# Kernel optimization log

Measured on AMD Instinct MI355X. Metric: run time of the kernel, lower is better.

The kernel has to match this reference:

```python
import jax, jax.numpy as jnp
import numpy as np

INPUT_SIZE = 32
HIDDEN_SIZE = 128
N_HEAD = 8
NER_NUMS = 8
D = INPUT_SIZE * NER_NUMS  # 256, attention feature dim per head


def setup_inputs() -> dict:
    key = jax.random.key(0)
    ks = jax.random.split(key, 10)
    B, S = 8, 2048
    x = jax.random.normal(ks[0], (B, S, D), dtype=jnp.float32)
    bi_lstm_o = jax.random.normal(ks[1], (B, S, 2 * HIDDEN_SIZE), dtype=jnp.float32)
    # per-head linear params, stacked on leading head axis (nn.init.normal_ -> std 1)
    Qw = jax.random.normal(ks[2], (N_HEAD, 2 * HIDDEN_SIZE, D), dtype=jnp.float32)
    Qb = jax.random.normal(ks[3], (N_HEAD, D), dtype=jnp.float32)
    Kw = jax.random.normal(ks[4], (N_HEAD, D, D), dtype=jnp.float32)
    Kb = jax.random.normal(ks[5], (N_HEAD, D), dtype=jnp.float32)
    Vw = jax.random.normal(ks[6], (N_HEAD, D, D), dtype=jnp.float32)
    Vb = jax.random.normal(ks[7], (N_HEAD, D), dtype=jnp.float32)
    Cw = jax.random.normal(ks[8], (N_HEAD * D, NER_NUMS), dtype=jnp.float32)
    Cb = jax.random.normal(ks[9], (NER_NUMS,), dtype=jnp.float32)
    return {"x": x, "bi_lstm_o": bi_lstm_o, "Qw": Qw, "Qb": Qb, "Kw": Kw,
            "Kb": Kb, "Vw": Vw, "Vb": Vb, "Cw": Cw, "Cb": Cb}


def reference(x, bi_lstm_o, Qw, Qb, Kw, Kb, Vw, Vb, Cw, Cb):
    # q from bi_lstm_o, k/v from x; all heads batched on axis h
    q = jnp.einsum('bsf,hfd->hbsd', bi_lstm_o, Qw) + Qb[:, None, None, :]
    k = jnp.einsum('bsf,hfd->hbsd', x, Kw) + Kb[:, None, None, :]
    v = jnp.einsum('bsf,hfd->hbsd', x, Vw) + Vb[:, None, None, :]
    scale = 1.0 / jnp.sqrt(jnp.float32(D))
    scores = jnp.einsum('hbsd,hbtd->hbst', q, k) * scale  # [H,B,S,S]
    attn = jax.nn.softmax(scores, axis=-1)
    o = jnp.einsum('hbst,hbtd->hbsd', attn, v)  # [H,B,S,D]
    B, S = x.shape[0], x.shape[1]
    concat = jnp.transpose(o, (1, 2, 0, 3)).reshape(B, S, N_HEAD * D)  # head order matches torch.cat
    return concat @ Cw + Cb
```

## Files before the change

kernel.cpp:

```cpp
#include <hip/hip_runtime.h>

#define H_ 8
#define B_ 8
#define S_ 2048
#define D_ 256

#define KSTRIDE 264
#define VSTRIDE 40
#define QTSTRIDE 136

typedef __attribute__((ext_vector_type(8))) _Float16 half8;
typedef __attribute__((ext_vector_type(4))) _Float16 half4v;
typedef __attribute__((ext_vector_type(2))) _Float16 half2v;
typedef __attribute__((ext_vector_type(4))) float f32x4;

__device__ inline void split8(const float* __restrict__ p, half8& hv, half8& lv) {
  float4 a = *(const float4*)p, b = *(const float4*)(p + 4);
  hv[0] = (_Float16)a.x; hv[1] = (_Float16)a.y; hv[2] = (_Float16)a.z; hv[3] = (_Float16)a.w;
  hv[4] = (_Float16)b.x; hv[5] = (_Float16)b.y; hv[6] = (_Float16)b.z; hv[7] = (_Float16)b.w;
  lv[0] = (_Float16)(a.x - (float)hv[0]); lv[1] = (_Float16)(a.y - (float)hv[1]);
  lv[2] = (_Float16)(a.z - (float)hv[2]); lv[3] = (_Float16)(a.w - (float)hv[3]);
  lv[4] = (_Float16)(b.x - (float)hv[4]); lv[5] = (_Float16)(b.y - (float)hv[5]);
  lv[6] = (_Float16)(b.z - (float)hv[6]); lv[7] = (_Float16)(b.w - (float)hv[7]);
}

__global__ void split_w_kernel(const float* __restrict__ W,
                               _Float16* __restrict__ thi, _Float16* __restrict__ tlo) {
  __shared__ float t[64][65];
  const int h = blockIdx.z, f0 = blockIdx.x * 64, d0 = blockIdx.y * 64;
  const int col = threadIdx.x & 63, rg = threadIdx.x >> 6;
#pragma unroll
  for (int it = 0; it < 16; ++it) {
    int f = rg * 16 + it;
    t[f][col] = W[((size_t)h * 256 + f0 + f) * 256 + d0 + col];
  }
  __syncthreads();
#pragma unroll
  for (int it = 0; it < 16; ++it) {
    int d = rg * 16 + it;
    float v = t[col][d];
    _Float16 hv = (_Float16)v;
    size_t idx = ((size_t)h * 256 + d0 + d) * 256 + f0 + col;
    thi[idx] = hv;
    tlo[idx] = (_Float16)(v - (float)hv);
  }
}

__global__ void out_init_kernel(float* __restrict__ out, const float* __restrict__ Cb) {
  int i = blockIdx.x * blockDim.x + threadIdx.x;
  if (i < B_ * S_ * 8) out[i] = Cb[i & 7];
}

template <int VMODE>
__global__ __launch_bounds__(256, 2) void proj_kernel(
    const float* __restrict__ A,
    const _Float16* __restrict__ Whi, const _Float16* __restrict__ Wlo,
    const float* __restrict__ bias, float oscale, int h0,
    _Float16* __restrict__ Ohi, _Float16* __restrict__ Olo) {
  constexpr bool TMULT = (VMODE != 1);
  __shared__ _Float16 a_hi[128 * VSTRIDE] __attribute__((aligned(16)));
  __shared__ _Float16 b_hi[128 * VSTRIDE] __attribute__((aligned(16)));
  __shared__ _Float16 a_lo[TMULT ? 128 * VSTRIDE : 8] __attribute__((aligned(16)));
  __shared__ _Float16 b_lo[TMULT ? 128 * VSTRIDE : 8] __attribute__((aligned(16)));
  const int tid = threadIdx.x;
  const int w = tid >> 6, lane = tid & 63;
  const int quad = lane >> 4, l15 = lane & 15;
  const int hb = blockIdx.z, h = h0 + (hb >> 3), b = hb & 7;
  const int s0 = blockIdx.x * 128, d0 = blockIdx.y * 128;
  const int wr = w >> 1, wc = w & 1;
  const f32x4 fz = {0.f, 0.f, 0.f, 0.f};
  f32x4 acc[4][4];
#pragma unroll
  for (int i = 0; i < 4; ++i)
#pragma unroll
    for (int j = 0; j < 4; ++j) acc[i][j] = fz;
  const size_t arow0 = (size_t)b * S_ + s0;
  const size_t wrow0 = (size_t)h * 256 + d0;
  for (int kk = 0; kk < 8; ++kk) {
    const int f0 = kk * 32;
    __syncthreads();
#pragma unroll
    for (int i = 0; i < 2; ++i) {
      int cc = i * 256 + tid;
      int r = cc >> 2, ch = (cc & 3) * 8;
      half8 hv, lv;
      split8(A + (arow0 + r) * 256 + f0 + ch, hv, lv);
      *(half8*)&a_hi[r * VSTRIDE + ch] = hv;
      size_t woff = (wrow0 + r) * 256 + f0 + ch;
      *(half8*)&b_hi[r * VSTRIDE + ch] = *(const half8*)(Whi + woff);
      if (TMULT) {
        *(half8*)&a_lo[r * VSTRIDE + ch] = lv;
        *(half8*)&b_lo[r * VSTRIDE + ch] = *(const half8*)(Wlo + woff);
      }
    }
    __syncthreads();
    half8 afh[4], afl[4], bfh[4], bfl[4];
#pragma unroll
    for (int t = 0; t < 4; ++t) {
      int ar = wr * 64 + t * 16 + l15;
      afh[t] = *(const half8*)&a_hi[ar * VSTRIDE + quad * 8];
      int br = wc * 64 + t * 16 + l15;
      bfh[t] = *(const half8*)&b_hi[br * VSTRIDE + quad * 8];
      if (TMULT) {
        afl[t] = *(const half8*)&a_lo[ar * VSTRIDE + quad * 8];
        bfl[t] = *(const half8*)&b_lo[br * VSTRIDE + quad * 8];
      }
    }
#pragma unroll
    for (int rf = 0; rf < 4; ++rf)
#pragma unroll
      for (int cf = 0; cf < 4; ++cf) {
        acc[rf][cf] = __builtin_amdgcn_mfma_f32_16x16x32_f16(afh[rf], bfh[cf], acc[rf][cf], 0, 0, 0);
        if (TMULT) {
          acc[rf][cf] = __builtin_amdgcn_mfma_f32_16x16x32_f16(afh[rf], bfl[cf], acc[rf][cf], 0, 0, 0);
          acc[rf][cf] = __builtin_amdgcn_mfma_f32_16x16x32_f16(afl[rf], bfh[cf], acc[rf][cf], 0, 0, 0);
        }
      }
  }
#pragma unroll
  for (int rf = 0; rf < 4; ++rf) {
#pragma unroll
    for (int cf = 0; cf < 4; ++cf) {
      const int d = d0 + wc * 64 + cf * 16 + l15;
      const float bv = bias[h * 256 + d];
      if (VMODE != 1) {
#pragma unroll
        for (int r = 0; r < 4; ++r) {
          const int s = s0 + wr * 64 + rf * 16 + quad * 4 + r;
          float val = (acc[rf][cf][r] + bv) * oscale;
          _Float16 hvv = (_Float16)val;
          size_t idx = ((size_t)hb * S_ + s) * 256 + d;
          Ohi[idx] = hvv;
          if (VMODE == 0) Olo[idx] = (_Float16)(val - (float)hvv);
        }
      } else {
        half4v pack;
#pragma unroll
        for (int r = 0; r < 4; ++r) pack[r] = (_Float16)((acc[rf][cf][r] + bv) * oscale);
        size_t idx = ((size_t)hb * 256 + d) * S_ + s0 + wr * 64 + rf * 16 + quad * 4;
        *(half4v*)(Ohi + idx) = pack;
      }
    }
  }
}

__device__ inline unsigned int pack2(float a, float b) {
  half2v h; h[0] = (_Float16)a; h[1] = (_Float16)b;
  return __builtin_bit_cast(unsigned int, h);
}

__global__ __launch_bounds__(256, 2) void flash_kernel(
    const float* __restrict__ bo,
    const _Float16* __restrict__ qwhi, const _Float16* __restrict__ qwlo,
    const float* __restrict__ qbias,
    const _Float16* __restrict__ khi,
    const _Float16* __restrict__ vt, const float* __restrict__ Cw,
    float* __restrict__ out, int h0) {
  __shared__ _Float16 khi_s[32 * KSTRIDE] __attribute__((aligned(16)));
  __shared__ _Float16 vt_s[256 * VSTRIDE] __attribute__((aligned(16)));
  __shared__ _Float16 wbuf[256 * VSTRIDE] __attribute__((aligned(16)));
  const int tid = threadIdx.x, w = tid >> 6, lane = tid & 63;
  const int quad = lane >> 4, l15 = lane & 15;
  const int hb = blockIdx.y, h = h0 + (hb >> 3), b = hb & 7;
  const int qbase = blockIdx.x * 64;

  const f32x4 fz = {0.f, 0.f, 0.f, 0.f};
  f32x4 qacc[16];
#pragma unroll
  for (int df = 0; df < 16; ++df) qacc[df] = fz;
  for (int kk = 0; kk < 8; ++kk) {
    __syncthreads();
#pragma unroll
    for (int i = 0; i < 4; ++i) {
      int c = i * 256 + tid;
      int dr = c >> 2, ch = (c & 3) * 8;
      size_t woff = ((size_t)h * 256 + dr) * 256 + kk * 32 + ch;
      *(half8*)&vt_s[dr * VSTRIDE + ch] = *(const half8*)(qwhi + woff);
      *(half8*)&wbuf[dr * VSTRIDE + ch] = *(const half8*)(qwlo + woff);
    }
    {
      int rrow = tid >> 2, ch = (tid & 3) * 8;
      half8 hv, lv;
      split8(bo + ((size_t)b * S_ + qbase + rrow) * 256 + kk * 32 + ch, hv, lv);
      *(half8*)&khi_s[rrow * VSTRIDE + ch] = hv;
      *(half8*)&khi_s[2560 + rrow * VSTRIDE + ch] = lv;
    }
    __syncthreads();
    half8 bh = *(const half8*)&khi_s[(w * 16 + l15) * VSTRIDE + quad * 8];
    half8 bl = *(const half8*)&khi_s[2560 + (w * 16 + l15) * VSTRIDE + quad * 8];
#pragma unroll
    for (int df = 0; df < 16; ++df) {
      half8 awh = *(const half8*)&vt_s[(df * 16 + l15) * VSTRIDE + quad * 8];
      half8 awl = *(const half8*)&wbuf[(df * 16 + l15) * VSTRIDE + quad * 8];
      qacc[df] = __builtin_amdgcn_mfma_f32_16x16x32_f16(awh, bh, qacc[df], 0, 0, 0);
      qacc[df] = __builtin_amdgcn_mfma_f32_16x16x32_f16(awl, bh, qacc[df], 0, 0, 0);
      qacc[df] = __builtin_amdgcn_mfma_f32_16x16x32_f16(awh, bl, qacc[df], 0, 0, 0);
    }
  }

  half8 stK[4], stV[4];
  auto LOADKV = [&](int kt) {
    size_t kbase = ((size_t)hb * S_ + (size_t)kt * 32) * 256;
#pragma unroll
    for (int i = 0; i < 4; ++i) {
      int cc = i * 256 + tid;
      int kr = cc >> 5, kch = (cc & 31) * 8;
      stK[i] = *(const half8*)(khi + kbase + kr * 256 + kch);
      int vd = cc >> 2, vch = (cc & 3) * 8;
      stV[i] = *(const half8*)(vt + ((size_t)hb * 256 + vd) * S_ + (size_t)kt * 32 + vch);
    }
  };
  LOADKV(0);

  half8 qfh[8], qfl[8];
#pragma unroll
  for (int ph = 0; ph < 4; ++ph) {
    const int dh = ph >> 1;
    const bool lo = ph & 1;
    __syncthreads();
#pragma unroll
    for (int dfi = 0; dfi < 8; ++dfi) {
      int df = dh * 8 + dfi;
#pragma unroll
      for (int rp = 0; rp < 2; ++rp) {
        half2v hw;
#pragma unroll
        for (int rr2 = 0; rr2 < 2; ++rr2) {
          int r = rp * 2 + rr2;
          float bv = qbias[h * 256 + df * 16 + quad * 4 + r];
          float val = (qacc[df][r] + bv) * 0.0625f;
          _Float16 hv = (_Float16)val;
          hw[rr2] = lo ? (_Float16)(val - (float)hv) : hv;
        }
        *(half2v*)&vt_s[(w * 16 + l15) * QTSTRIDE + dfi * 16 + quad * 4 + rp * 2] = hw;
      }
    }
    __syncthreads();
#pragma unroll
    for (int k2 = 0; k2 < 4; ++k2) {
      half8 v = *(const half8*)&vt_s[(w * 16 + l15) * QTSTRIDE + k2 * 32 + quad * 8];
      if (lo) qfl[dh * 4 + k2] = v;
      else    qfh[dh * 4 + k2] = v;
    }
  }

  f32x4 o_acc[16];
#pragma unroll
  for (int df = 0; df < 16; ++df) o_acc[df] = fz;
  float m_r = -3.0e38f, l_r = 0.f;

  for (int kt = 0; kt < 64; ++kt) {
    __syncthreads();
#pragma unroll
    for (int i = 0; i < 4; ++i) {
      int cc = i * 256 + tid;
      int kr = cc >> 5, kch = (cc & 31) * 8;
      *(half8*)&khi_s[kr * KSTRIDE + kch] = stK[i];
      int vd = cc >> 2, vch = (cc & 3) * 8;
      *(half8*)&vt_s[vd * VSTRIDE + vch] = stV[i];
    }
    __syncthreads();
    if (kt < 63) LOADKV(kt + 1);
    f32x4 sc0 = fz, sc1 = fz;
#pragma unroll
    for (int ks = 0; ks < 8; ++ks) {
      half8 bh0 = *(const half8*)&khi_s[(0 * 16 + l15) * KSTRIDE + ks * 32 + quad * 8];
      sc0 = __builtin_amdgcn_mfma_f32_16x16x32_f16(bh0, qfh[ks], sc0, 0, 0, 0);
      sc0 = __builtin_amdgcn_mfma_f32_16x16x32_f16(bh0, qfl[ks], sc0, 0, 0, 0);
      half8 bh1 = *(const half8*)&khi_s[(1 * 16 + l15) * KSTRIDE + ks * 32 + quad * 8];
      sc1 = __builtin_amdgcn_mfma_f32_16x16x32_f16(bh1, qfh[ks], sc1, 0, 0, 0);
      sc1 = __builtin_amdgcn_mfma_f32_16x16x32_f16(bh1, qfl[ks], sc1, 0, 0, 0);
    }
    float v = fmaxf(fmaxf(fmaxf(sc0[0], sc0[1]), fmaxf(sc0[2], sc0[3])),
                    fmaxf(fmaxf(sc1[0], sc1[1]), fmaxf(sc1[2], sc1[3])));
    v = fmaxf(v, __shfl_xor(v, 16));
    v = fmaxf(v, __shfl_xor(v, 32));
    if (__any(v > m_r + 8.0f)) {
      const float mn = fmaxf(m_r, v);
      const float al = __expf(m_r - mn);
      m_r = mn;
      l_r *= al;
      float al_r[4];
#pragma unroll
      for (int r = 0; r < 4; ++r) al_r[r] = __shfl(al, quad * 4 + r);
#pragma unroll
      for (int df = 0; df < 16; ++df)
#pragma unroll
        for (int r = 0; r < 4; ++r) o_acc[df][r] *= al_r[r];
    }
    float p0[4], p1[4], s = 0.f;
#pragma unroll
    for (int r = 0; r < 4; ++r) {
      p0[r] = __expf(sc0[r] - m_r);
      p1[r] = __expf(sc1[r] - m_r);
      s += p0[r] + p1[r];
    }
    s += __shfl_xor(s, 16);
    s += __shfl_xor(s, 32);
    l_r += s;
    {
      unsigned int u0 = pack2(p0[0], p0[1]), u1 = pack2(p0[2], p0[3]);
      unsigned int v0 = pack2(p1[0], p1[1]), v1 = pack2(p1[2], p1[3]);
      const int src0 = ((quad & 1) << 5) + l15;
      const int src1 = src0 + 16;
      unsigned int a0 = __shfl(u0, src0), a1 = __shfl(u1, src0);
      unsigned int a2 = __shfl(u0, src1), a3 = __shfl(u1, src1);
      unsigned int c0 = __shfl(v0, src0), c1 = __shfl(v1, src0);
      unsigned int c2 = __shfl(v0, src1), c3 = __shfl(v1, src1);
      union U { unsigned int u[4]; half8 h; } pu;
      const bool hiq = quad >= 2;
      pu.u[0] = hiq ? c0 : a0;
      pu.u[1] = hiq ? c1 : a1;
      pu.u[2] = hiq ? c2 : a2;
      pu.u[3] = hiq ? c3 : a3;
      half8 pf = pu.h;
#pragma unroll
      for (int df = 0; df < 16; ++df) {
        half8 vf = *(const half8*)&vt_s[(df * 16 + l15) * VSTRIDE + quad * 8];
        o_acc[df] = __builtin_amdgcn_mfma_f32_16x16x32_f16(pf, vf, o_acc[df], 0, 0, 0);
      }
    }
  }
  float rcl[4];
#pragma unroll
  for (int r = 0; r < 4; ++r) rcl[r] = 1.0f / __shfl(l_r, quad * 4 + r);
  float part[32];
#pragma unroll
  for (int i = 0; i < 32; ++i) part[i] = 0.f;
#pragma unroll
  for (int df = 0; df < 16; ++df) {
    const float4* cwv = (const float4*)(Cw + ((size_t)h * 256 + df * 16 + l15) * 8);
    float4 c0 = cwv[0], c1 = cwv[1];
#pragma unroll
    for (int r = 0; r < 4; ++r) {
      float ov = o_acc[df][r] * rcl[r];
      part[r * 8 + 0] += ov * c0.x;
      part[r * 8 + 1] += ov * c0.y;
      part[r * 8 + 2] += ov * c0.z;
      part[r * 8 + 3] += ov * c0.w;
      part[r * 8 + 4] += ov * c1.x;
      part[r * 8 + 5] += ov * c1.y;
      part[r * 8 + 6] += ov * c1.z;
      part[r * 8 + 7] += ov * c1.w;
    }
  }
#pragma unroll
  for (int i = 0; i < 32; ++i) {
    float v = part[i];
    v += __shfl_xor(v, 1);
    v += __shfl_xor(v, 2);
    v += __shfl_xor(v, 4);
    v += __shfl_xor(v, 8);
    part[i] = v;
  }
  if (l15 == 0) {
#pragma unroll
    for (int r = 0; r < 4; ++r) {
      int s = qbase + w * 16 + quad * 4 + r;
#pragma unroll
      for (int j = 0; j < 8; ++j)
        atomicAdd(&out[((size_t)b * S_ + s) * 8 + j], part[r * 8 + j]);
    }
  }
}

extern "C" void kernel_launch(void* const* d_in, const int* in_sizes, int n_in,
                              void* d_out, int out_size, void* d_ws, size_t ws_size,
                              hipStream_t stream) {
  const float* x  = (const float*)d_in[0];
  const float* bo = (const float*)d_in[1];
  const float* Qw = (const float*)d_in[2];
  const float* Qb = (const float*)d_in[3];
  const float* Kw = (const float*)d_in[4];
  const float* Kb = (const float*)d_in[5];
  const float* Vw = (const float*)d_in[6];
  const float* Vb = (const float*)d_in[7];
  const float* Cw = (const float*)d_in[8];
  const float* Cb = (const float*)d_in[9];
  float* out = (float*)d_out;

  const size_t NW  = (size_t)H_ * 256 * 256;
  const size_t NHB = (size_t)B_ * S_ * 256;
  const size_t ALN = 256;
  auto pad = [](size_t b) { return (b + 255) & ~(size_t)255; };

  int HC = 8;
  while (HC > 1) {
    size_t need = 6 * pad(NW * 2) + 2 * pad((size_t)HC * NHB * 2) + ALN;
    if (need <= ws_size) break;
    HC >>= 1;
  }

  char* base = (char*)d_ws;
  size_t off = 0;
  auto carve = [&](size_t nelem) -> _Float16* {
    _Float16* p = (_Float16*)(base + off);
    off += pad(nelem * 2);
    return p;
  };
  _Float16* qwt_hi = carve(NW); _Float16* qwt_lo = carve(NW);
  _Float16* kwt_hi = carve(NW); _Float16* kwt_lo = carve(NW);
  _Float16* vwt_hi = carve(NW); _Float16* vwt_lo = carve(NW);
  const size_t NC = (size_t)HC * NHB;
  _Float16* k_hi = carve(NC);
  _Float16* v_t  = carve(NC);

  dim3 wg(4, 4, 8);
  split_w_kernel<<<wg, 256, 0, stream>>>(Qw, qwt_hi, qwt_lo);
  split_w_kernel<<<wg, 256, 0, stream>>>(Kw, kwt_hi, kwt_lo);
  split_w_kernel<<<wg, 256, 0, stream>>>(Vw, vwt_hi, vwt_lo);
  out_init_kernel<<<(B_ * S_ * 8) / 256, 256, 0, stream>>>(out, Cb);

  for (int h0 = 0; h0 < H_; h0 += HC) {
    dim3 pg(16, 2, HC * 8);
    proj_kernel<2><<<pg, 256, 0, stream>>>(x, kwt_hi, kwt_lo, Kb, 1.0f, h0, k_hi, nullptr);
    proj_kernel<1><<<pg, 256, 0, stream>>>(x, vwt_hi, vwt_lo, Vb, 1.0f, h0, v_t, nullptr);
    dim3 fg(32, HC * 8);
    flash_kernel<<<fg, 256, 0, stream>>>(bo, qwt_hi, qwt_lo, Qb, k_hi, v_t, Cw, out, h0);
  }
}
```

Before: 777.9 us.

## Double-buffer K/V tiles in LDS with one barrier per iteration

Replaces the separate shared arrays with one unified LDS buffer and double-buffers the K and V tiles. Each iteration writes the next tile into the alternate buffer while computing on the current one, and prefetches two tiles ahead from global memory. This cuts the two barriers per key tile down to one and overlaps LDS stores with MFMA work. LDS use grows from about 55KB to about 73KB per block, which may limit the two-blocks-per-CU target, and staging registers now live longer.

```diff
diff --git a/kernel.cpp b/kernel.cpp
--- a/kernel.cpp
+++ b/kernel.cpp
@@ -156,9 +156,12 @@
     const _Float16* __restrict__ khi,
     const _Float16* __restrict__ vt, const float* __restrict__ Cw,
     float* __restrict__ out, int h0) {
-  __shared__ _Float16 khi_s[32 * KSTRIDE] __attribute__((aligned(16)));
-  __shared__ _Float16 vt_s[256 * VSTRIDE] __attribute__((aligned(16)));
-  __shared__ _Float16 wbuf[256 * VSTRIDE] __attribute__((aligned(16)));
+  __shared__ _Float16 smem[37376] __attribute__((aligned(16)));
+  _Float16* qw_hi = smem + 8448;
+  _Float16* qw_lo = smem + 27136;
+  _Float16* bo_hi = smem;
+  _Float16* bo_lo = smem + 2560;
+  _Float16* qtb   = smem + 8448;
   const int tid = threadIdx.x, w = tid >> 6, lane = tid & 63;
   const int quad = lane >> 4, l15 = lane & 15;
   const int hb = blockIdx.y, h = h0 + (hb >> 3), b = hb & 7;
@@ -175,23 +178,23 @@
       int c = i * 256 + tid;
       int dr = c >> 2, ch = (c & 3) * 8;
       size_t woff = ((size_t)h * 256 + dr) * 256 + kk * 32 + ch;
-      *(half8*)&vt_s[dr * VSTRIDE + ch] = *(const half8*)(qwhi + woff);
-      *(half8*)&wbuf[dr * VSTRIDE + ch] = *(const half8*)(qwlo + woff);
+      *(half8*)&qw_hi[dr * VSTRIDE + ch] = *(const half8*)(qwhi + woff);
+      *(half8*)&qw_lo[dr * VSTRIDE + ch] = *(const half8*)(qwlo + woff);
     }
     {
       int rrow = tid >> 2, ch = (tid & 3) * 8;
       half8 hv, lv;
       split8(bo + ((size_t)b * S_ + qbase + rrow) * 256 + kk * 32 + ch, hv, lv);
-      *(half8*)&khi_s[rrow * VSTRIDE + ch] = hv;
-      *(half8*)&khi_s[2560 + rrow * VSTRIDE + ch] = lv;
-    }
-    __syncthreads();
-    half8 bh = *(const half8*)&khi_s[(w * 16 + l15) * VSTRIDE + quad * 8];
-    half8 bl = *(const half8*)&khi_s[2560 + (w * 16 + l15) * VSTRIDE + quad * 8];
+      *(half8*)&bo_hi[rrow * VSTRIDE + ch] = hv;
+      *(half8*)&bo_lo[rrow * VSTRIDE + ch] = lv;
+    }
+    __syncthreads();
+    half8 bh = *(const half8*)&bo_hi[(w * 16 + l15) * VSTRIDE + quad * 8];
+    half8 bl = *(const half8*)&bo_lo[(w * 16 + l15) * VSTRIDE + quad * 8];
 #pragma unroll
     for (int df = 0; df < 16; ++df) {
-      half8 awh = *(const half8*)&vt_s[(df * 16 + l15) * VSTRIDE + quad * 8];
-      half8 awl = *(const half8*)&wbuf[(df * 16 + l15) * VSTRIDE + quad * 8];
+      half8 awh = *(const half8*)&qw_hi[(df * 16 + l15) * VSTRIDE + quad * 8];
+      half8 awl = *(const half8*)&qw_lo[(df * 16 + l15) * VSTRIDE + quad * 8];
       qacc[df] = __builtin_amdgcn_mfma_f32_16x16x32_f16(awh, bh, qacc[df], 0, 0, 0);
       qacc[df] = __builtin_amdgcn_mfma_f32_16x16x32_f16(awl, bh, qacc[df], 0, 0, 0);
       qacc[df] = __builtin_amdgcn_mfma_f32_16x16x32_f16(awh, bl, qacc[df], 0, 0, 0);
@@ -232,17 +235,29 @@
           _Float16 hv = (_Float16)val;
           hw[rr2] = lo ? (_Float16)(val - (float)hv) : hv;
         }
-        *(half2v*)&vt_s[(w * 16 + l15) * QTSTRIDE + dfi * 16 + quad * 4 + rp * 2] = hw;
+        *(half2v*)&qtb[(w * 16 + l15) * QTSTRIDE + dfi * 16 + quad * 4 + rp * 2] = hw;
       }
     }
     __syncthreads();
 #pragma unroll
     for (int k2 = 0; k2 < 4; ++k2) {
-      half8 v = *(const half8*)&vt_s[(w * 16 + l15) * QTSTRIDE + k2 * 32 + quad * 8];
+      half8 v = *(const half8*)&qtb[(w * 16 + l15) * QTSTRIDE + k2 * 32 + quad * 8];
       if (lo) qfl[dh * 4 + k2] = v;
       else    qfh[dh * 4 + k2] = v;
     }
   }
+  __syncthreads();
+
+#pragma unroll
+  for (int i = 0; i < 4; ++i) {
+    int cc = i * 256 + tid;
+    int kr = cc >> 5, kch = (cc & 31) * 8;
+    *(half8*)&smem[kr * KSTRIDE + kch] = stK[i];
+    int vd = cc >> 2, vch = (cc & 3) * 8;
+    *(half8*)&smem[8448 + vd * VSTRIDE + vch] = stV[i];
+  }
+  LOADKV(1);
+  __syncthreads();
 
   f32x4 o_acc[16];
 #pragma unroll
@@ -250,24 +265,28 @@
   float m_r = -3.0e38f, l_r = 0.f;
 
   for (int kt = 0; kt < 64; ++kt) {
-    __syncthreads();
-#pragma unroll
-    for (int i = 0; i < 4; ++i) {
-      int cc = i * 256 + tid;
-      int kr = cc >> 5, kch = (cc & 31) * 8;
-      *(half8*)&khi_s[kr * KSTRIDE + kch] = stK[i];
-      int vd = cc >> 2, vch = (cc & 3) * 8;
-      *(half8*)&vt_s[vd * VSTRIDE + vch] = stV[i];
-    }
-    __syncthreads();
-    if (kt < 63) LOADKV(kt + 1);
+    _Float16* kbuf = smem + (kt & 1) * 18688;
+    _Float16* vbuf = kbuf + 8448;
+    if (kt < 63) {
+      _Float16* kw = smem + ((kt + 1) & 1) * 18688;
+      _Float16* vw = kw + 8448;
+#pragma unroll
+      for (int i = 0; i < 4; ++i) {
+        int cc = i * 256 + tid;
+        int kr = cc >> 5, kch = (cc & 31) * 8;
+        *(half8*)&kw[kr * KSTRIDE + kch] = stK[i];
+        int vd = cc >> 2, vch = (cc & 3) * 8;
+        *(half8*)&vw[vd * VSTRIDE + vch] = stV[i];
+      }
+      if (kt < 62) LOADKV(kt + 2);
+    }
     f32x4 sc0 = fz, sc1 = fz;
 #pragma unroll
     for (int ks = 0; ks < 8; ++ks) {
-      half8 bh0 = *(const half8*)&khi_s[(0 * 16 + l15) * KSTRIDE + ks * 32 + quad * 8];
+      half8 bh0 = *(const half8*)&kbuf[(0 * 16 + l15) * KSTRIDE + ks * 32 + quad * 8];
       sc0 = __builtin_amdgcn_mfma_f32_16x16x32_f16(bh0, qfh[ks], sc0, 0, 0, 0);
       sc0 = __builtin_amdgcn_mfma_f32_16x16x32_f16(bh0, qfl[ks], sc0, 0, 0, 0);
-      half8 bh1 = *(const half8*)&khi_s[(1 * 16 + l15) * KSTRIDE + ks * 32 + quad * 8];
+      half8 bh1 = *(const half8*)&kbuf[(1 * 16 + l15) * KSTRIDE + ks * 32 + quad * 8];
       sc1 = __builtin_amdgcn_mfma_f32_16x16x32_f16(bh1, qfh[ks], sc1, 0, 0, 0);
       sc1 = __builtin_amdgcn_mfma_f32_16x16x32_f16(bh1, qfl[ks], sc1, 0, 0, 0);
     }
@@ -316,10 +335,11 @@
       half8 pf = pu.h;
 #pragma unroll
       for (int df = 0; df < 16; ++df) {
-        half8 vf = *(const half8*)&vt_s[(df * 16 + l15) * VSTRIDE + quad * 8];
+        half8 vf = *(const half8*)&vbuf[(df * 16 + l15) * VSTRIDE + quad * 8];
         o_acc[df] = __builtin_amdgcn_mfma_f32_16x16x32_f16(pf, vf, o_acc[df], 0, 0, 0);
       }
     }
+    __syncthreads();
   }
   float rcl[4];
 #pragma unroll
```

After: 807.3 us. 3.8% more time.
